# Performance work log

Measured on AMD Instinct MI355X. Metric: run time of the kernel, lower is better.

## Reference

```python
import jax, jax.numpy as jnp
from jax import lax
import numpy as np

B, T, F, U, O = 512, 512, 128, 256, 32  # batch, max_t, joint feature dim, lstm units, n_output


def setup_inputs() -> dict:
    key = jax.random.key(0)
    k = jax.random.split(key, 6)
    return {
        "x_joint": jax.random.normal(k[0], (B, T, F), dtype=jnp.float32),
        "Wx": jax.random.normal(k[1], (F, 4 * U), dtype=jnp.float32) / np.sqrt(F).astype(np.float32),
        "Wh": jax.random.normal(k[2], (U, 4 * U), dtype=jnp.float32) / np.sqrt(U).astype(np.float32),
        "b": jnp.zeros((4 * U,), dtype=jnp.float32),
        "Wo": jax.random.normal(k[3], (U, O), dtype=jnp.float32) / np.sqrt(U).astype(np.float32),
        "bo": jnp.zeros((O,), dtype=jnp.float32),
        "seq_lengths": jax.random.randint(k[4], (B,), 0, T, dtype=jnp.int32),
    }


def reference(x_joint, Wx, Wh, b, Wo, bo, seq_lengths):
    """Masked LSTM decoder scan with per-step Dense projection.

    Flax nn.RNN(DecoderLSTMCell): LSTMCell gates i,f,g,o then Dense(n_output).
    With return_carry=True + seq_lengths, flax only uses seq_lengths to slice the
    final carry, which RNNSurrogate discards; outputs are the full per-step
    predictions, so seq_lengths does not enter the returned math.
    """
    bsz, t, _ = x_joint.shape
    units = Wh.shape[0]
    # precompute input contribution to all 4 gates: [B, T, 4U]
    x_proj = jnp.einsum('btf,fg->btg', x_joint, Wx) + b
    c0 = jnp.zeros((bsz, units), dtype=x_joint.dtype)
    h0 = jnp.zeros((bsz, units), dtype=x_joint.dtype)

    def step(carry, xt):
        c, h = carry
        z = xt + h @ Wh  # [B, 4U]
        i, f, g, o = jnp.split(z, 4, axis=-1)
        c = jax.nn.sigmoid(f) * c + jax.nn.sigmoid(i) * jnp.tanh(g)
        h = jax.nn.sigmoid(o) * jnp.tanh(c)
        y = h @ Wo + bo  # per-step Dense projection
        return (c, h), y

    _, ys = lax.scan(step, (c0, h0), x_proj.transpose(1, 0, 2))  # ys: [T, B, O]
    return ys.transpose(1, 0, 2)  # [B, T, O]
```

## Files before the change

### kernel.cpp

```cpp
#include <hip/hip_runtime.h>
#include <stdint.h>

#define BB 512
#define TT 512
#define FF 128
#define UU 256

typedef float f32x4 __attribute__((ext_vector_type(4)));
typedef short short8 __attribute__((ext_vector_type(8)));
typedef int int4v __attribute__((ext_vector_type(4)));
typedef float float4v __attribute__((ext_vector_type(4)));
typedef unsigned short ushort4v __attribute__((ext_vector_type(4)));

__device__ __forceinline__ unsigned short f2bf(float f) {
  union { float f; uint32_t u; } v; v.f = f;
  uint32_t u = v.u;
  u += 0x7fffu + ((u >> 16) & 1u);
  return (unsigned short)(u >> 16);
}
__device__ __forceinline__ float fast_rcp(float x) { return __builtin_amdgcn_rcpf(x); }
__device__ __forceinline__ float sigmoidf_(float x) { return fast_rcp(1.f + __expf(-x)); }
__device__ __forceinline__ float tanhf_(float x) { return 1.f - 2.f * fast_rcp(1.f + __expf(2.f * x)); }

__global__ void prep_w(const float* __restrict__ Wx, const float* __restrict__ Wh,
                       const float* __restrict__ Wo,
                       unsigned short* __restrict__ Wt, unsigned short* __restrict__ Wot,
                       int* __restrict__ flags) {
  int bidx = blockIdx.x;
  int tid = threadIdx.x;
  if (bidx < 1024) {
    int n = bidx, k = tid;
    float v = (k < FF) ? Wx[(size_t)k * 1024 + n] : Wh[(size_t)(k - FF) * 1024 + n];
    Wt[(size_t)n * 384 + k] = f2bf(v);
  } else if (bidx == 1024) {
    for (int i = tid; i < 32 * 256; i += 384) {
      int o = i >> 8, u = i & 255;
      Wot[o * 256 + u] = f2bf(Wo[(size_t)u * 32 + o]);
    }
  } else {
    for (int i = tid; i < 64 * 32; i += 384)
      __hip_atomic_store(&flags[i], 0, __ATOMIC_RELAXED, __HIP_MEMORY_SCOPE_SYSTEM);
  }
}

__global__ void conv_x(const float* __restrict__ xf, unsigned short* __restrict__ xb) {
  size_t i = (size_t)blockIdx.x * 1024 + (size_t)threadIdx.x * 4;
  float4v v = *(const float4v*)(xf + i);
  ushort4v o;
  o.x = f2bf(v.x); o.y = f2bf(v.y); o.z = f2bf(v.z); o.w = f2bf(v.w);
  *(ushort4v*)(xb + i) = o;
}

__device__ __forceinline__ short8 load_xfrag(const unsigned short* p) {
  return *(const short8*)p;
}
__device__ __forceinline__ short8 load_xfrag(const float* p) {
  float4v lo = *(const float4v*)p;
  float4v hi = *(const float4v*)(p + 4);
  union { short8 v; unsigned short s[8]; } a;
  a.s[0] = f2bf(lo.x); a.s[1] = f2bf(lo.y); a.s[2] = f2bf(lo.z); a.s[3] = f2bf(lo.w);
  a.s[4] = f2bf(hi.x); a.s[5] = f2bf(hi.y); a.s[6] = f2bf(hi.z); a.s[7] = f2bf(hi.w);
  return a.v;
}

__device__ __forceinline__ void load4_coh(const unsigned short* p,
                                          short8& q0, short8& q1, short8& q2, short8& q3) {
  int4v a0, a1, a2, a3;
  asm volatile(
      "global_load_dwordx4 %0, %4, off sc0 sc1\n\t"
      "global_load_dwordx4 %1, %4, off offset:64 sc0 sc1\n\t"
      "global_load_dwordx4 %2, %4, off offset:128 sc0 sc1\n\t"
      "global_load_dwordx4 %3, %4, off offset:192 sc0 sc1\n\t"
      "s_waitcnt vmcnt(0)"
      : "=&v"(a0), "=&v"(a1), "=&v"(a2), "=&v"(a3) : "v"(p) : "memory");
  __builtin_amdgcn_sched_barrier(0);
  q0 = __builtin_bit_cast(short8, a0);
  q1 = __builtin_bit_cast(short8, a1);
  q2 = __builtin_bit_cast(short8, a2);
  q3 = __builtin_bit_cast(short8, a3);
}
__device__ __forceinline__ void store_coh_u16(unsigned short* p, unsigned short v) {
  asm volatile("global_store_short %0, %1, off sc0 sc1" :: "v"(p), "v"((uint32_t)v) : "memory");
}

template <int HALF, typename XT>
__device__ __forceinline__ void lstm_core(const XT* __restrict__ x,
                                          const unsigned short* __restrict__ Wt,
                                          const float* __restrict__ bvec,
                                          unsigned short* __restrict__ h_hist,
                                          int* flags, int bid, char* lds) {
  const int mt = bid & 31;
  const int partner = bid ^ 32;
  const int tid = threadIdx.x;
  const int w = tid >> 6, l = tid & 63;
  const int lr = l & 15, lhi = l >> 4;
  const int b0 = mt * 16;
  const int uloc = HALF * 128 + w * 16 + lr;
  char* hlds = lds + 131072;

#pragma unroll
  for (int g = 0; g < 4; ++g)
#pragma unroll
    for (int kk = 0; kk < 4; ++kk) {
      const unsigned short* wp = Wt + (size_t)(g * 256 + uloc) * 384 + kk * 32 + 8 * lhi;
      *(short8*)(lds + ((size_t)((w * 16 + g * 4 + kk) * 64 + l)) * 16) = *(const short8*)wp;
    }

  short8 Bh[4][8];
#pragma unroll
  for (int g = 0; g < 4; ++g) {
    const unsigned short* wp = Wt + (size_t)(g * 256 + uloc) * 384 + FF + 8 * lhi;
#pragma unroll
    for (int kf = 0; kf < 8; ++kf) Bh[g][kf] = *(const short8*)(wp + kf * 32);
  }
  float bias[4];
#pragma unroll
  for (int g = 0; g < 4; ++g) bias[g] = bvec[g * 256 + uloc];
  float cst[4] = {0.f, 0.f, 0.f, 0.f};

  constexpr int kf_own = HALF * 4;
  constexpr int kf_par = (1 - HALF) * 4;
  constexpr int kh_par = (1 - HALF) * 128;

  const int* fp = flags + partner * 32;

  short8 xa[4];
  {
    const XT* xp = x + ((size_t)(b0 + lr) * TT + 0) * FF + 8 * lhi;
#pragma unroll
    for (int kk = 0; kk < 4; ++kk) xa[kk] = load_xfrag(xp + kk * 32);
  }
  __syncthreads();

#pragma unroll 1
  for (int t = 0; t < TT; ++t) {
    const int cur = t & 1, nxt = cur ^ 1;

    f32x4 acc[4];
#pragma unroll
    for (int g = 0; g < 4; ++g) { f32x4 a4 = {bias[g], bias[g], bias[g], bias[g]}; acc[g] = a4; }

    if (t > 0) {
      short8 ho[4];
#pragma unroll
      for (int ko = 0; ko < 4; ++ko) {
        const int byte = cur * 4096 + lr * 256 + ((ko * 64 + lhi * 16) ^ ((lr & 7) << 4));
        ho[ko] = *(const short8*)(hlds + byte);
      }
#pragma unroll
      for (int ko = 0; ko < 4; ++ko)
#pragma unroll
        for (int g = 0; g < 4; ++g)
          acc[g] = __builtin_amdgcn_mfma_f32_16x16x32_bf16(ho[ko], Bh[g][kf_own + ko], acc[g], 0, 0, 0);
    }

#pragma unroll
    for (int kk = 0; kk < 4; ++kk) {
      short8 bx[4];
#pragma unroll
      for (int g = 0; g < 4; ++g)
        bx[g] = *(const short8*)(lds + ((size_t)((w * 16 + g * 4 + kk) * 64 + l)) * 16);
#pragma unroll
      for (int g = 0; g < 4; ++g)
        acc[g] = __builtin_amdgcn_mfma_f32_16x16x32_bf16(xa[kk], bx[g], acc[g], 0, 0, 0);
    }

    {
      const int tn = (t + 1 < TT) ? t + 1 : t;
      const XT* xp = x + ((size_t)(b0 + lr) * TT + tn) * FF + 8 * lhi;
#pragma unroll
      for (int kk = 0; kk < 4; ++kk) xa[kk] = load_xfrag(xp + kk * 32);
    }

    if (t > 0) {
      int fv;
      do {
        asm volatile("global_load_dword %0, %1, off sc0 sc1\n\ts_waitcnt vmcnt(0)"
                     : "=v"(fv) : "v"(fp) : "memory");
      } while (fv < t);
      __builtin_amdgcn_sched_barrier(0);

      const unsigned short* hpp =
          h_hist + (size_t)t * (BB * UU) + (size_t)(b0 + lr) * UU + 8 * lhi + kh_par;
      short8 hq0, hq1, hq2, hq3;
      load4_coh(hpp, hq0, hq1, hq2, hq3);
#pragma unroll
      for (int g = 0; g < 4; ++g) acc[g] = __builtin_amdgcn_mfma_f32_16x16x32_bf16(hq0, Bh[g][kf_par + 0], acc[g], 0, 0, 0);
#pragma unroll
      for (int g = 0; g < 4; ++g) acc[g] = __builtin_amdgcn_mfma_f32_16x16x32_bf16(hq1, Bh[g][kf_par + 1], acc[g], 0, 0, 0);
#pragma unroll
      for (int g = 0; g < 4; ++g) acc[g] = __builtin_amdgcn_mfma_f32_16x16x32_bf16(hq2, Bh[g][kf_par + 2], acc[g], 0, 0, 0);
#pragma unroll
      for (int g = 0; g < 4; ++g) acc[g] = __builtin_amdgcn_mfma_f32_16x16x32_bf16(hq3, Bh[g][kf_par + 3], acc[g], 0, 0, 0);
    }

    unsigned short hs[4];
#pragma unroll
    for (int r = 0; r < 4; ++r) {
      float zi = acc[0][r], zf = acc[1][r], zg = acc[2][r], zo = acc[3][r];
      float si = sigmoidf_(zi), sf = sigmoidf_(zf), so = sigmoidf_(zo);
      float tg = tanhf_(zg);
      float cn = sf * cst[r] + si * tg;
      cst[r] = cn;
      hs[r] = f2bf(so * tanhf_(cn));
    }

    unsigned short* hw = h_hist + (size_t)(t + 1) * (BB * UU) + uloc;
#pragma unroll
    for (int r = 0; r < 4; ++r) {
      const int row = 4 * lhi + r;
      const int byte = nxt * 4096 + row * 256 + (((w * 16 + lr) * 2) ^ ((row & 7) << 4));
      *(unsigned short*)(hlds + byte) = hs[r];
      store_coh_u16(hw + (size_t)(b0 + row) * UU, hs[r]);
    }

    asm volatile("s_waitcnt vmcnt(0)" ::: "memory");
    __syncthreads();
    if (tid == 0)
      __hip_atomic_store(&flags[bid * 32], t + 1, __ATOMIC_RELAXED, __HIP_MEMORY_SCOPE_SYSTEM);
  }
}

template <typename XT>
__global__ void __launch_bounds__(512, 2)
lstm_main7(const XT* __restrict__ x, const unsigned short* __restrict__ Wt,
           const float* __restrict__ bvec, unsigned short* __restrict__ h_hist, int* flags) {
  __shared__ __align__(16) char lds[139264];
  const int bid = blockIdx.x;
  if (bid < 32) lstm_core<0, XT>(x, Wt, bvec, h_hist, flags, bid, lds);
  else          lstm_core<1, XT>(x, Wt, bvec, h_hist, flags, bid, lds);
}

__global__ void __launch_bounds__(256)
y_gemm(const unsigned short* __restrict__ h_hist, const unsigned short* __restrict__ Wot,
       const float* __restrict__ bo, float* __restrict__ out) {
  int gw = (int)((blockIdx.x * 256 + threadIdx.x) >> 6);
  int l = threadIdx.x & 63;
  int lr = l & 15, lhi = l >> 4;
  int b = gw >> 5;
  int t0 = (gw & 31) * 16;

  short8 Wf[2][8];
#pragma unroll
  for (int n = 0; n < 2; ++n) {
    const unsigned short* wp = Wot + (n * 16 + lr) * 256 + 8 * lhi;
#pragma unroll
    for (int kk = 0; kk < 8; ++kk) Wf[n][kk] = *(const short8*)(wp + kk * 32);
  }
  f32x4 acc[2];
#pragma unroll
  for (int n = 0; n < 2; ++n) {
    float bb = bo[n * 16 + lr];
    f32x4 a4 = {bb, bb, bb, bb};
    acc[n] = a4;
  }
  const unsigned short* hp =
      h_hist + ((size_t)(t0 + lr + 1) * BB + b) * UU + 8 * lhi;
#pragma unroll
  for (int kk = 0; kk < 8; ++kk) {
    short8 a = *(const short8*)(hp + kk * 32);
#pragma unroll
    for (int n = 0; n < 2; ++n)
      acc[n] = __builtin_amdgcn_mfma_f32_16x16x32_bf16(a, Wf[n][kk], acc[n], 0, 0, 0);
  }
#pragma unroll
  for (int n = 0; n < 2; ++n) {
    int o = n * 16 + lr;
#pragma unroll
    for (int r = 0; r < 4; ++r) {
      int t = t0 + 4 * lhi + r;
      out[((size_t)b * TT + t) * 32 + o] = acc[n][r];
    }
  }
}

extern "C" void kernel_launch(void* const* d_in, const int* in_sizes, int n_in,
                              void* d_out, int out_size, void* d_ws, size_t ws_size,
                              hipStream_t stream) {
  const float* x  = (const float*)d_in[0];
  const float* Wx = (const float*)d_in[1];
  const float* Wh = (const float*)d_in[2];
  const float* bv = (const float*)d_in[3];
  const float* Wo = (const float*)d_in[4];
  const float* bo = (const float*)d_in[5];

  char* ws = (char*)d_ws;
  size_t off = 0;
  unsigned short* h_hist = (unsigned short*)(ws + off); off += (size_t)513 * BB * UU * 2;
  unsigned short* Wt384  = (unsigned short*)(ws + off); off += (size_t)1024 * 384 * 2;
  unsigned short* Wot    = (unsigned short*)(ws + off); off += (size_t)32 * 256 * 2;
  int* flags             = (int*)(ws + off);            off += (size_t)64 * 32 * 4;
  off = (off + 255) & ~(size_t)255;
  unsigned short* xb = (unsigned short*)(ws + off);
  const size_t need_xb = off + (size_t)BB * TT * FF * 2;

  prep_w<<<1026, 384, 0, stream>>>(Wx, Wh, Wo, Wt384, Wot, flags);
  if (ws_size >= need_xb) {
    conv_x<<<32768, 256, 0, stream>>>(x, xb);
    lstm_main7<unsigned short><<<64, 512, 0, stream>>>(xb, Wt384, bv, h_hist, flags);
  } else {
    lstm_main7<float><<<64, 512, 0, stream>>>(x, Wt384, bv, h_hist, flags);
  }
  y_gemm<<<4096, 256, 0, stream>>>(h_hist, Wot, bo, (float*)d_out);
}
```

Before: 1.799 ms.

## Embed step tags in exchanged h values, fuse output projection into LSTM

Partner blocks now exchange hidden state through a small double-buffered scratch area. Each 32-bit word packs a bf16 h value with the step number, so the consumer polls the data itself instead of waiting on a separate flag and then reading h_hist. This removes one round-trip of global latency per step, along with the trailing vmcnt wait and barrier-before-flag. The input projection for the next step is computed after the h store so it overlaps the partner's latency. The output Dense projection is fused into the recurrent kernel, which eliminates the full h history buffer and the separate y_gemm launch. The trade-off is double the exchange bytes (32-bit words instead of 16-bit) and extra MFMA work inside the serial loop.

```diff
diff --git a/kernel.cpp b/kernel.cpp
--- a/kernel.cpp
+++ b/kernel.cpp
@@ -25,7 +25,7 @@
 __global__ void prep_w(const float* __restrict__ Wx, const float* __restrict__ Wh,
                        const float* __restrict__ Wo,
                        unsigned short* __restrict__ Wt, unsigned short* __restrict__ Wot,
-                       int* __restrict__ flags) {
+                       int* __restrict__ xch) {
   int bidx = blockIdx.x;
   int tid = threadIdx.x;
   if (bidx < 1024) {
@@ -38,8 +38,8 @@
       Wot[o * 256 + u] = f2bf(Wo[(size_t)u * 32 + o]);
     }
   } else {
-    for (int i = tid; i < 64 * 32; i += 384)
-      __hip_atomic_store(&flags[i], 0, __ATOMIC_RELAXED, __HIP_MEMORY_SCOPE_SYSTEM);
+    int base = (bidx - 1025) * 2048;
+    for (int i = tid; i < 2048; i += 384) xch[base + i] = 0;
   }
 }
 
@@ -63,40 +63,63 @@
   return a.v;
 }
 
-__device__ __forceinline__ void load4_coh(const unsigned short* p,
-                                          short8& q0, short8& q1, short8& q2, short8& q3) {
-  int4v a0, a1, a2, a3;
-  asm volatile(
-      "global_load_dwordx4 %0, %4, off sc0 sc1\n\t"
-      "global_load_dwordx4 %1, %4, off offset:64 sc0 sc1\n\t"
-      "global_load_dwordx4 %2, %4, off offset:128 sc0 sc1\n\t"
-      "global_load_dwordx4 %3, %4, off offset:192 sc0 sc1\n\t"
-      "s_waitcnt vmcnt(0)"
-      : "=&v"(a0), "=&v"(a1), "=&v"(a2), "=&v"(a3) : "v"(p) : "memory");
+__device__ __forceinline__ void store_sc01(int* p, int v) {
+  asm volatile("global_store_dword %0, %1, off sc0 sc1" :: "v"(p), "v"(v) : "memory");
+}
+__device__ __forceinline__ int tchk(const int4v& v, int t) {
+  return ((v.x ^ t) | (v.y ^ t) | (v.z ^ t) | (v.w ^ t)) & 0xffff;
+}
+__device__ __forceinline__ uint32_t pk2(int lo, int hi) {
+  return ((uint32_t)lo >> 16) | ((uint32_t)hi & 0xffff0000u);
+}
+__device__ __forceinline__ short8 pack2(const int4v& a, const int4v& b) {
+  int4v k;
+  k.x = (int)pk2(a.x, a.y); k.y = (int)pk2(a.z, a.w);
+  k.z = (int)pk2(b.x, b.y); k.w = (int)pk2(b.z, b.w);
+  return __builtin_bit_cast(short8, k);
+}
+
+__device__ __forceinline__ void poll_hq(const int* pb, int t, short8* hq) {
+  int4v a0, a1, a2, a3, a4, a5, a6, a7;
+  for (;;) {
+    asm volatile(
+        "global_load_dwordx4 %0, %8, off sc0 sc1\n\t"
+        "global_load_dwordx4 %1, %8, off offset:16 sc0 sc1\n\t"
+        "global_load_dwordx4 %2, %8, off offset:128 sc0 sc1\n\t"
+        "global_load_dwordx4 %3, %8, off offset:144 sc0 sc1\n\t"
+        "global_load_dwordx4 %4, %8, off offset:256 sc0 sc1\n\t"
+        "global_load_dwordx4 %5, %8, off offset:272 sc0 sc1\n\t"
+        "global_load_dwordx4 %6, %8, off offset:384 sc0 sc1\n\t"
+        "global_load_dwordx4 %7, %8, off offset:400 sc0 sc1\n\t"
+        "s_waitcnt vmcnt(0)"
+        : "=&v"(a0), "=&v"(a1), "=&v"(a2), "=&v"(a3),
+          "=&v"(a4), "=&v"(a5), "=&v"(a6), "=&v"(a7)
+        : "v"(pb) : "memory");
+    int m = tchk(a0, t) | tchk(a1, t) | tchk(a2, t) | tchk(a3, t)
+          | tchk(a4, t) | tchk(a5, t) | tchk(a6, t) | tchk(a7, t);
+    if (__all(m == 0)) break;
+  }
   __builtin_amdgcn_sched_barrier(0);
-  q0 = __builtin_bit_cast(short8, a0);
-  q1 = __builtin_bit_cast(short8, a1);
-  q2 = __builtin_bit_cast(short8, a2);
-  q3 = __builtin_bit_cast(short8, a3);
-}
-__device__ __forceinline__ void store_coh_u16(unsigned short* p, unsigned short v) {
-  asm volatile("global_store_short %0, %1, off sc0 sc1" :: "v"(p), "v"((uint32_t)v) : "memory");
+  hq[0] = pack2(a0, a1); hq[1] = pack2(a2, a3);
+  hq[2] = pack2(a4, a5); hq[3] = pack2(a6, a7);
 }
 
 template <int HALF, typename XT>
 __device__ __forceinline__ void lstm_core(const XT* __restrict__ x,
                                           const unsigned short* __restrict__ Wt,
+                                          const unsigned short* __restrict__ Wot,
                                           const float* __restrict__ bvec,
-                                          unsigned short* __restrict__ h_hist,
-                                          int* flags, int bid, char* lds) {
+                                          const float* __restrict__ bo,
+                                          float* __restrict__ out,
+                                          int* __restrict__ xch, int bid, char* lds) {
   const int mt = bid & 31;
-  const int partner = bid ^ 32;
   const int tid = threadIdx.x;
   const int w = tid >> 6, l = tid & 63;
   const int lr = l & 15, lhi = l >> 4;
   const int b0 = mt * 16;
   const int uloc = HALF * 128 + w * 16 + lr;
-  char* hlds = lds + 131072;
+  char* h_lds  = lds + 131072;
+  char* wo_lds = lds + 139264;
 
 #pragma unroll
   for (int g = 0; g < 4; ++g)
@@ -105,6 +128,13 @@
       const unsigned short* wp = Wt + (size_t)(g * 256 + uloc) * 384 + kk * 32 + 8 * lhi;
       *(short8*)(lds + ((size_t)((w * 16 + g * 4 + kk) * 64 + l)) * 16) = *(const short8*)wp;
     }
+  if (w == 0) {
+#pragma unroll
+    for (int kf = 0; kf < 8; ++kf) {
+      const unsigned short* wp = Wot + (size_t)(HALF * 16 + lr) * 256 + kf * 32 + 8 * lhi;
+      *(short8*)(wo_lds + (size_t)(kf * 64 + l) * 16) = *(const short8*)wp;
+    }
+  }
 
   short8 Bh[4][8];
 #pragma unroll
@@ -116,21 +146,33 @@
   float bias[4];
 #pragma unroll
   for (int g = 0; g < 4; ++g) bias[g] = bvec[g * 256 + uloc];
+  const float bob = bo[HALF * 16 + lr];
   float cst[4] = {0.f, 0.f, 0.f, 0.f};
 
-  constexpr int kf_own = HALF * 4;
-  constexpr int kf_par = (1 - HALF) * 4;
-  constexpr int kh_par = (1 - HALF) * 128;
-
-  const int* fp = flags + partner * 32;
-
-  short8 xa[4];
+  const int rtile = (mt * 2 + (1 - HALF)) * 2;
+  const int wtile = (mt * 2 + HALF) * 2;
+  const int roff = lr * 128 + 8 * lhi;
+
+  f32x4 zx[4];
   {
+    short8 xa0[4];
     const XT* xp = x + ((size_t)(b0 + lr) * TT + 0) * FF + 8 * lhi;
 #pragma unroll
-    for (int kk = 0; kk < 4; ++kk) xa[kk] = load_xfrag(xp + kk * 32);
-  }
-  __syncthreads();
+    for (int kk = 0; kk < 4; ++kk) xa0[kk] = load_xfrag(xp + kk * 32);
+    __syncthreads();
+#pragma unroll
+    for (int g = 0; g < 4; ++g) { f32x4 a4 = {bias[g], bias[g], bias[g], bias[g]}; zx[g] = a4; }
+#pragma unroll
+    for (int kk = 0; kk < 4; ++kk) {
+      short8 bx[4];
+#pragma unroll
+      for (int g = 0; g < 4; ++g)
+        bx[g] = *(const short8*)(lds + ((size_t)((w * 16 + g * 4 + kk) * 64 + l)) * 16);
+#pragma unroll
+      for (int g = 0; g < 4; ++g)
+        zx[g] = __builtin_amdgcn_mfma_f32_16x16x32_bf16(xa0[kk], bx[g], zx[g], 0, 0, 0);
+    }
+  }
 
 #pragma unroll 1
   for (int t = 0; t < TT; ++t) {
@@ -138,60 +180,35 @@
 
     f32x4 acc[4];
 #pragma unroll
-    for (int g = 0; g < 4; ++g) { f32x4 a4 = {bias[g], bias[g], bias[g], bias[g]}; acc[g] = a4; }
-
-    if (t > 0) {
-      short8 ho[4];
-#pragma unroll
-      for (int ko = 0; ko < 4; ++ko) {
-        const int byte = cur * 4096 + lr * 256 + ((ko * 64 + lhi * 16) ^ ((lr & 7) << 4));
-        ho[ko] = *(const short8*)(hlds + byte);
-      }
-#pragma unroll
-      for (int ko = 0; ko < 4; ++ko)
-#pragma unroll
-        for (int g = 0; g < 4; ++g)
-          acc[g] = __builtin_amdgcn_mfma_f32_16x16x32_bf16(ho[ko], Bh[g][kf_own + ko], acc[g], 0, 0, 0);
-    }
-
-#pragma unroll
-    for (int kk = 0; kk < 4; ++kk) {
-      short8 bx[4];
-#pragma unroll
-      for (int g = 0; g < 4; ++g)
-        bx[g] = *(const short8*)(lds + ((size_t)((w * 16 + g * 4 + kk) * 64 + l)) * 16);
-#pragma unroll
-      for (int g = 0; g < 4; ++g)
-        acc[g] = __builtin_amdgcn_mfma_f32_16x16x32_bf16(xa[kk], bx[g], acc[g], 0, 0, 0);
-    }
-
+    for (int g = 0; g < 4; ++g) acc[g] = zx[g];
+
+    short8 xan[4];
     {
       const int tn = (t + 1 < TT) ? t + 1 : t;
       const XT* xp = x + ((size_t)(b0 + lr) * TT + tn) * FF + 8 * lhi;
 #pragma unroll
-      for (int kk = 0; kk < 4; ++kk) xa[kk] = load_xfrag(xp + kk * 32);
-    }
-
+      for (int kk = 0; kk < 4; ++kk) xan[kk] = load_xfrag(xp + kk * 32);
+    }
+
+    short8 ho[4], hq[4];
     if (t > 0) {
-      int fv;
-      do {
-        asm volatile("global_load_dword %0, %1, off sc0 sc1\n\ts_waitcnt vmcnt(0)"
-                     : "=v"(fv) : "v"(fp) : "memory");
-      } while (fv < t);
-      __builtin_amdgcn_sched_barrier(0);
-
-      const unsigned short* hpp =
-          h_hist + (size_t)t * (BB * UU) + (size_t)(b0 + lr) * UU + 8 * lhi + kh_par;
-      short8 hq0, hq1, hq2, hq3;
-      load4_coh(hpp, hq0, hq1, hq2, hq3);
-#pragma unroll
-      for (int g = 0; g < 4; ++g) acc[g] = __builtin_amdgcn_mfma_f32_16x16x32_bf16(hq0, Bh[g][kf_par + 0], acc[g], 0, 0, 0);
-#pragma unroll
-      for (int g = 0; g < 4; ++g) acc[g] = __builtin_amdgcn_mfma_f32_16x16x32_bf16(hq1, Bh[g][kf_par + 1], acc[g], 0, 0, 0);
-#pragma unroll
-      for (int g = 0; g < 4; ++g) acc[g] = __builtin_amdgcn_mfma_f32_16x16x32_bf16(hq2, Bh[g][kf_par + 2], acc[g], 0, 0, 0);
-#pragma unroll
-      for (int g = 0; g < 4; ++g) acc[g] = __builtin_amdgcn_mfma_f32_16x16x32_bf16(hq3, Bh[g][kf_par + 3], acc[g], 0, 0, 0);
+#pragma unroll
+      for (int ko = 0; ko < 4; ++ko) {
+        const int byte = cur * 4096 + lr * 256 + ((ko * 64 + lhi * 16) ^ ((lr & 7) << 4));
+        ho[ko] = *(const short8*)(h_lds + byte);
+      }
+#pragma unroll
+      for (int ko = 0; ko < 4; ++ko)
+#pragma unroll
+        for (int g = 0; g < 4; ++g)
+          acc[g] = __builtin_amdgcn_mfma_f32_16x16x32_bf16(ho[ko], Bh[g][HALF * 4 + ko], acc[g], 0, 0, 0);
+
+      poll_hq(xch + (rtile + cur) * 2048 + roff, t, hq);
+#pragma unroll
+      for (int kf = 0; kf < 4; ++kf)
+#pragma unroll
+        for (int g = 0; g < 4; ++g)
+          acc[g] = __builtin_amdgcn_mfma_f32_16x16x32_bf16(hq[kf], Bh[g][(1 - HALF) * 4 + kf], acc[g], 0, 0, 0);
     }
 
     unsigned short hs[4];
@@ -205,73 +222,81 @@
       hs[r] = f2bf(so * tanhf_(cn));
     }
 
-    unsigned short* hw = h_hist + (size_t)(t + 1) * (BB * UU) + uloc;
+    const int wb = (wtile + nxt) * 2048 + w * 16 + lr;
 #pragma unroll
     for (int r = 0; r < 4; ++r) {
       const int row = 4 * lhi + r;
       const int byte = nxt * 4096 + row * 256 + (((w * 16 + lr) * 2) ^ ((row & 7) << 4));
-      *(unsigned short*)(hlds + byte) = hs[r];
-      store_coh_u16(hw + (size_t)(b0 + row) * UU, hs[r]);
-    }
-
-    asm volatile("s_waitcnt vmcnt(0)" ::: "memory");
+      *(unsigned short*)(h_lds + byte) = hs[r];
+      store_sc01(xch + wb + row * 128, ((int)(uint32_t)hs[r] << 16) | (t + 1));
+    }
+
+#pragma unroll
+    for (int g = 0; g < 4; ++g) { f32x4 a4 = {bias[g], bias[g], bias[g], bias[g]}; zx[g] = a4; }
+#pragma unroll
+    for (int kk = 0; kk < 4; ++kk) {
+      short8 bx[4];
+#pragma unroll
+      for (int g = 0; g < 4; ++g)
+        bx[g] = *(const short8*)(lds + ((size_t)((w * 16 + g * 4 + kk) * 64 + l)) * 16);
+#pragma unroll
+      for (int g = 0; g < 4; ++g)
+        zx[g] = __builtin_amdgcn_mfma_f32_16x16x32_bf16(xan[kk], bx[g], zx[g], 0, 0, 0);
+    }
+    if (t > 0) {
+      f32x4 yacc = {bob, bob, bob, bob};
+#pragma unroll
+      for (int ko = 0; ko < 4; ++ko) {
+        short8 wo = *(const short8*)(wo_lds + (size_t)((HALF * 4 + ko) * 64 + l) * 16);
+        yacc = __builtin_amdgcn_mfma_f32_16x16x32_bf16(ho[ko], wo, yacc, 0, 0, 0);
+      }
+#pragma unroll
+      for (int kf = 0; kf < 4; ++kf) {
+        short8 wo = *(const short8*)(wo_lds + (size_t)(((1 - HALF) * 4 + kf) * 64 + l) * 16);
+        yacc = __builtin_amdgcn_mfma_f32_16x16x32_bf16(hq[kf], wo, yacc, 0, 0, 0);
+      }
+#pragma unroll
+      for (int r = 0; r < 4; ++r)
+        out[((size_t)(b0 + 4 * lhi + r) * TT + (t - 1)) * 32 + HALF * 16 + lr] = yacc[r];
+    }
+
     __syncthreads();
-    if (tid == 0)
-      __hip_atomic_store(&flags[bid * 32], t + 1, __ATOMIC_RELAXED, __HIP_MEMORY_SCOPE_SYSTEM);
+  }
+
+  {
+    short8 ho[4], hq[4];
+#pragma unroll
+    for (int ko = 0; ko < 4; ++ko) {
+      const int byte = 0 * 4096 + lr * 256 + ((ko * 64 + lhi * 16) ^ ((lr & 7) << 4));
+      ho[ko] = *(const short8*)(h_lds + byte);
+    }
+    poll_hq(xch + (rtile + 0) * 2048 + roff, TT, hq);
+    f32x4 yacc = {bob, bob, bob, bob};
+#pragma unroll
+    for (int ko = 0; ko < 4; ++ko) {
+      short8 wo = *(const short8*)(wo_lds + (size_t)((HALF * 4 + ko) * 64 + l) * 16);
+      yacc = __builtin_amdgcn_mfma_f32_16x16x32_bf16(ho[ko], wo, yacc, 0, 0, 0);
+    }
+#pragma unroll
+    for (int kf = 0; kf < 4; ++kf) {
+      short8 wo = *(const short8*)(wo_lds + (size_t)(((1 - HALF) * 4 + kf) * 64 + l) * 16);
+      yacc = __builtin_amdgcn_mfma_f32_16x16x32_bf16(hq[kf], wo, yacc, 0, 0, 0);
+    }
+#pragma unroll
+    for (int r = 0; r < 4; ++r)
+      out[((size_t)(b0 + 4 * lhi + r) * TT + (TT - 1)) * 32 + HALF * 16 + lr] = yacc[r];
   }
 }
 
 template <typename XT>
 __global__ void __launch_bounds__(512, 2)
-lstm_main7(const XT* __restrict__ x, const unsigned short* __restrict__ Wt,
-           const float* __restrict__ bvec, unsigned short* __restrict__ h_hist, int* flags) {
-  __shared__ __align__(16) char lds[139264];
+lstm_main8(const XT* __restrict__ x, const unsigned short* __restrict__ Wt,
+           const unsigned short* __restrict__ Wot, const float* __restrict__ bvec,
+           const float* __restrict__ bo, float* __restrict__ out, int* __restrict__ xch) {
+  __shared__ __align__(16) char lds[147456];
   const int bid = blockIdx.x;
-  if (bid < 32) lstm_core<0, XT>(x, Wt, bvec, h_hist, flags, bid, lds);
-  else          lstm_core<1, XT>(x, Wt, bvec, h_hist, flags, bid, lds);
-}
-
-__global__ void __launch_bounds__(256)
-y_gemm(const unsigned short* __restrict__ h_hist, const unsigned short* __restrict__ Wot,
-       const float* __restrict__ bo, float* __restrict__ out) {
-  int gw = (int)((blockIdx.x * 256 + threadIdx.x) >> 6);
-  int l = threadIdx.x & 63;
-  int lr = l & 15, lhi = l >> 4;
-  int b = gw >> 5;
-  int t0 = (gw & 31) * 16;
-
-  short8 Wf[2][8];
-#pragma unroll
-  for (int n = 0; n < 2; ++n) {
-    const unsigned short* wp = Wot + (n * 16 + lr) * 256 + 8 * lhi;
-#pragma unroll
-    for (int kk = 0; kk < 8; ++kk) Wf[n][kk] = *(const short8*)(wp + kk * 32);
-  }
-  f32x4 acc[2];
-#pragma unroll
-  for (int n = 0; n < 2; ++n) {
-    float bb = bo[n * 16 + lr];
-    f32x4 a4 = {bb, bb, bb, bb};
-    acc[n] = a4;
-  }
-  const unsigned short* hp =
-      h_hist + ((size_t)(t0 + lr + 1) * BB + b) * UU + 8 * lhi;
-#pragma unroll
-  for (int kk = 0; kk < 8; ++kk) {
-    short8 a = *(const short8*)(hp + kk * 32);
-#pragma unroll
-    for (int n = 0; n < 2; ++n)
-      acc[n] = __builtin_amdgcn_mfma_f32_16x16x32_bf16(a, Wf[n][kk], acc[n], 0, 0, 0);
-  }
-#pragma unroll
-  for (int n = 0; n < 2; ++n) {
-    int o = n * 16 + lr;
-#pragma unroll
-    for (int r = 0; r < 4; ++r) {
-      int t = t0 + 4 * lhi + r;
-      out[((size_t)b * TT + t) * 32 + o] = acc[n][r];
-    }
-  }
+  if (bid < 32) lstm_core<0, XT>(x, Wt, Wot, bvec, bo, out, xch, bid, lds);
+  else          lstm_core<1, XT>(x, Wt, Wot, bvec, bo, out, xch, bid, lds);
 }
 
 extern "C" void kernel_launch(void* const* d_in, const int* in_sizes, int n_in,
@@ -286,20 +311,18 @@
 
   char* ws = (char*)d_ws;
   size_t off = 0;
-  unsigned short* h_hist = (unsigned short*)(ws + off); off += (size_t)513 * BB * UU * 2;
-  unsigned short* Wt384  = (unsigned short*)(ws + off); off += (size_t)1024 * 384 * 2;
-  unsigned short* Wot    = (unsigned short*)(ws + off); off += (size_t)32 * 256 * 2;
-  int* flags             = (int*)(ws + off);            off += (size_t)64 * 32 * 4;
+  int* xch = (int*)(ws + off);                          off += (size_t)262144 * 4;
+  unsigned short* Wt384 = (unsigned short*)(ws + off);  off += (size_t)1024 * 384 * 2;
+  unsigned short* Wot   = (unsigned short*)(ws + off);  off += (size_t)32 * 256 * 2;
   off = (off + 255) & ~(size_t)255;
   unsigned short* xb = (unsigned short*)(ws + off);
   const size_t need_xb = off + (size_t)BB * TT * FF * 2;
 
-  prep_w<<<1026, 384, 0, stream>>>(Wx, Wh, Wo, Wt384, Wot, flags);
+  prep_w<<<1153, 384, 0, stream>>>(Wx, Wh, Wo, Wt384, Wot, xch);
   if (ws_size >= need_xb) {
     conv_x<<<32768, 256, 0, stream>>>(x, xb);
-    lstm_main7<unsigned short><<<64, 512, 0, stream>>>(xb, Wt384, bv, h_hist, flags);
+    lstm_main8<unsigned short><<<64, 512, 0, stream>>>(xb, Wt384, Wot, bv, bo, (float*)d_out, xch);
   } else {
-    lstm_main7<float><<<64, 512, 0, stream>>>(x, Wt384, bv, h_hist, flags);
-  }
-  y_gemm<<<4096, 256, 0, stream>>>(h_hist, Wot, bo, (float*)d_out);
-}
+    lstm_main8<float><<<64, 512, 0, stream>>>(x, Wt384, Wot, bv, bo, (float*)d_out, xch);
+  }
+}
```

Result: slower. 3.324 ms (+84.8%).

## Replace flag-based partner sync with tagged hidden-state exchange buffer

Applied to the files above, without the earlier changes.

Removes the separate per-block flag and the wait for store completion before signalling. Each hidden value is now written as a 32-bit word that packs the bf16 value with the step number into a double-buffered exchange area. The partner block polls that data directly until every tag matches the current step, then stages the values through LDS to build MFMA fragments. This cuts a full store-drain plus flag round trip from each step, in exchange for wider polling loads, an extra LDS pass and barrier, and reliance on tag correctness with 16-bit step counters.

```diff
diff --git a/kernel.cpp b/kernel.cpp
--- a/kernel.cpp
+++ b/kernel.cpp
@@ -25,7 +25,7 @@
 __global__ void prep_w(const float* __restrict__ Wx, const float* __restrict__ Wh,
                        const float* __restrict__ Wo,
                        unsigned short* __restrict__ Wt, unsigned short* __restrict__ Wot,
-                       int* __restrict__ flags) {
+                       int* __restrict__ xch) {
   int bidx = blockIdx.x;
   int tid = threadIdx.x;
   if (bidx < 1024) {
@@ -38,8 +38,8 @@
       Wot[o * 256 + u] = f2bf(Wo[(size_t)u * 32 + o]);
     }
   } else {
-    for (int i = tid; i < 64 * 32; i += 384)
-      __hip_atomic_store(&flags[i], 0, __ATOMIC_RELAXED, __HIP_MEMORY_SCOPE_SYSTEM);
+    int base = (bidx - 1025) * 2048;
+    for (int i = tid; i < 2048; i += 384) xch[base + i] = 0;
   }
 }
 
@@ -63,24 +63,11 @@
   return a.v;
 }
 
-__device__ __forceinline__ void load4_coh(const unsigned short* p,
-                                          short8& q0, short8& q1, short8& q2, short8& q3) {
-  int4v a0, a1, a2, a3;
-  asm volatile(
-      "global_load_dwordx4 %0, %4, off sc0 sc1\n\t"
-      "global_load_dwordx4 %1, %4, off offset:64 sc0 sc1\n\t"
-      "global_load_dwordx4 %2, %4, off offset:128 sc0 sc1\n\t"
-      "global_load_dwordx4 %3, %4, off offset:192 sc0 sc1\n\t"
-      "s_waitcnt vmcnt(0)"
-      : "=&v"(a0), "=&v"(a1), "=&v"(a2), "=&v"(a3) : "v"(p) : "memory");
-  __builtin_amdgcn_sched_barrier(0);
-  q0 = __builtin_bit_cast(short8, a0);
-  q1 = __builtin_bit_cast(short8, a1);
-  q2 = __builtin_bit_cast(short8, a2);
-  q3 = __builtin_bit_cast(short8, a3);
-}
-__device__ __forceinline__ void store_coh_u16(unsigned short* p, unsigned short v) {
-  asm volatile("global_store_short %0, %1, off sc0 sc1" :: "v"(p), "v"((uint32_t)v) : "memory");
+__device__ __forceinline__ void store_sc01(int* p, int v) {
+  asm volatile("global_store_dword %0, %1, off sc0 sc1" :: "v"(p), "v"(v) : "memory");
+}
+__device__ __forceinline__ uint32_t pk2(int lo, int hi) {
+  return ((uint32_t)lo >> 16) | ((uint32_t)hi & 0xffff0000u);
 }
 
 template <int HALF, typename XT>
@@ -88,15 +75,15 @@
                                           const unsigned short* __restrict__ Wt,
                                           const float* __restrict__ bvec,
                                           unsigned short* __restrict__ h_hist,
-                                          int* flags, int bid, char* lds) {
+                                          int* __restrict__ xch, int bid, char* lds) {
   const int mt = bid & 31;
-  const int partner = bid ^ 32;
   const int tid = threadIdx.x;
   const int w = tid >> 6, l = tid & 63;
   const int lr = l & 15, lhi = l >> 4;
   const int b0 = mt * 16;
   const int uloc = HALF * 128 + w * 16 + lr;
   char* hlds = lds + 131072;
+  char* plds = lds + 139264;
 
 #pragma unroll
   for (int g = 0; g < 4; ++g)
@@ -120,9 +107,12 @@
 
   constexpr int kf_own = HALF * 4;
   constexpr int kf_par = (1 - HALF) * 4;
-  constexpr int kh_par = (1 - HALF) * 128;
-
-  const int* fp = flags + partner * 32;
+
+  const int rtile = (mt * 2 + (1 - HALF)) * 2;
+  const int wtile = (mt * 2 + HALF) * 2;
+
+  const int prow = tid >> 5;
+  const int pwbyte = (prow * 256 + (tid & 31) * 8) ^ ((prow & 7) << 4);
 
   short8 xa[4];
   {
@@ -173,25 +163,31 @@
     }
 
     if (t > 0) {
-      int fv;
-      do {
-        asm volatile("global_load_dword %0, %1, off sc0 sc1\n\ts_waitcnt vmcnt(0)"
-                     : "=v"(fv) : "v"(fp) : "memory");
-      } while (fv < t);
+      const int* pp = xch + (rtile + cur) * 2048 + 4 * tid;
+      int4v a;
+      for (;;) {
+        asm volatile("global_load_dwordx4 %0, %1, off sc0 sc1\n\ts_waitcnt vmcnt(0)"
+                     : "=&v"(a) : "v"(pp) : "memory");
+        int m = ((a.x ^ t) | (a.y ^ t) | (a.z ^ t) | (a.w ^ t)) & 0xffff;
+        if (__all(m == 0)) break;
+      }
       __builtin_amdgcn_sched_barrier(0);
 
-      const unsigned short* hpp =
-          h_hist + (size_t)t * (BB * UU) + (size_t)(b0 + lr) * UU + 8 * lhi + kh_par;
-      short8 hq0, hq1, hq2, hq3;
-      load4_coh(hpp, hq0, hq1, hq2, hq3);
-#pragma unroll
-      for (int g = 0; g < 4; ++g) acc[g] = __builtin_amdgcn_mfma_f32_16x16x32_bf16(hq0, Bh[g][kf_par + 0], acc[g], 0, 0, 0);
-#pragma unroll
-      for (int g = 0; g < 4; ++g) acc[g] = __builtin_amdgcn_mfma_f32_16x16x32_bf16(hq1, Bh[g][kf_par + 1], acc[g], 0, 0, 0);
-#pragma unroll
-      for (int g = 0; g < 4; ++g) acc[g] = __builtin_amdgcn_mfma_f32_16x16x32_bf16(hq2, Bh[g][kf_par + 2], acc[g], 0, 0, 0);
-#pragma unroll
-      for (int g = 0; g < 4; ++g) acc[g] = __builtin_amdgcn_mfma_f32_16x16x32_bf16(hq3, Bh[g][kf_par + 3], acc[g], 0, 0, 0);
+      uint32_t d0 = pk2(a.x, a.y), d1 = pk2(a.z, a.w);
+      *(uint64_t*)(plds + pwbyte) = ((uint64_t)d1 << 32) | d0;
+      __syncthreads();
+
+      short8 hq[4];
+#pragma unroll
+      for (int ko = 0; ko < 4; ++ko) {
+        const int byte = (lr * 256 + lhi * 16 + ko * 64) ^ ((lr & 7) << 4);
+        hq[ko] = *(const short8*)(plds + byte);
+      }
+#pragma unroll
+      for (int ko = 0; ko < 4; ++ko)
+#pragma unroll
+        for (int g = 0; g < 4; ++g)
+          acc[g] = __builtin_amdgcn_mfma_f32_16x16x32_bf16(hq[ko], Bh[g][kf_par + ko], acc[g], 0, 0, 0);
     }
 
     unsigned short hs[4];
@@ -205,30 +201,30 @@
       hs[r] = f2bf(so * tanhf_(cn));
     }
 
+    const int wb = (wtile + nxt) * 2048 + w * 16 + lr;
     unsigned short* hw = h_hist + (size_t)(t + 1) * (BB * UU) + uloc;
 #pragma unroll
     for (int r = 0; r < 4; ++r) {
       const int row = 4 * lhi + r;
       const int byte = nxt * 4096 + row * 256 + (((w * 16 + lr) * 2) ^ ((row & 7) << 4));
       *(unsigned short*)(hlds + byte) = hs[r];
-      store_coh_u16(hw + (size_t)(b0 + row) * UU, hs[r]);
-    }
-
-    asm volatile("s_waitcnt vmcnt(0)" ::: "memory");
+      store_sc01(xch + wb + row * 128, ((int)(uint32_t)hs[r] << 16) | (t + 1));
+      hw[(size_t)(b0 + row) * UU] = hs[r];
+    }
+
     __syncthreads();
-    if (tid == 0)
-      __hip_atomic_store(&flags[bid * 32], t + 1, __ATOMIC_RELAXED, __HIP_MEMORY_SCOPE_SYSTEM);
   }
 }
 
 template <typename XT>
 __global__ void __launch_bounds__(512, 2)
-lstm_main7(const XT* __restrict__ x, const unsigned short* __restrict__ Wt,
-           const float* __restrict__ bvec, unsigned short* __restrict__ h_hist, int* flags) {
-  __shared__ __align__(16) char lds[139264];
+lstm_main10(const XT* __restrict__ x, const unsigned short* __restrict__ Wt,
+            const float* __restrict__ bvec, unsigned short* __restrict__ h_hist,
+            int* __restrict__ xch) {
+  __shared__ __align__(16) char lds[143360];
   const int bid = blockIdx.x;
-  if (bid < 32) lstm_core<0, XT>(x, Wt, bvec, h_hist, flags, bid, lds);
-  else          lstm_core<1, XT>(x, Wt, bvec, h_hist, flags, bid, lds);
+  if (bid < 32) lstm_core<0, XT>(x, Wt, bvec, h_hist, xch, bid, lds);
+  else          lstm_core<1, XT>(x, Wt, bvec, h_hist, xch, bid, lds);
 }
 
 __global__ void __launch_bounds__(256)
@@ -286,20 +282,20 @@
 
   char* ws = (char*)d_ws;
   size_t off = 0;
+  int* xch = (int*)(ws + off);                          off += (size_t)262144 * 4;
   unsigned short* h_hist = (unsigned short*)(ws + off); off += (size_t)513 * BB * UU * 2;
   unsigned short* Wt384  = (unsigned short*)(ws + off); off += (size_t)1024 * 384 * 2;
   unsigned short* Wot    = (unsigned short*)(ws + off); off += (size_t)32 * 256 * 2;
-  int* flags             = (int*)(ws + off);            off += (size_t)64 * 32 * 4;
   off = (off + 255) & ~(size_t)255;
   unsigned short* xb = (unsigned short*)(ws + off);
   const size_t need_xb = off + (size_t)BB * TT * FF * 2;
 
-  prep_w<<<1026, 384, 0, stream>>>(Wx, Wh, Wo, Wt384, Wot, flags);
+  prep_w<<<1153, 384, 0, stream>>>(Wx, Wh, Wo, Wt384, Wot, xch);
   if (ws_size >= need_xb) {
     conv_x<<<32768, 256, 0, stream>>>(x, xb);
-    lstm_main7<unsigned short><<<64, 512, 0, stream>>>(xb, Wt384, bv, h_hist, flags);
+    lstm_main10<unsigned short><<<64, 512, 0, stream>>>(xb, Wt384, bv, h_hist, xch);
   } else {
-    lstm_main7<float><<<64, 512, 0, stream>>>(x, Wt384, bv, h_hist, flags);
+    lstm_main10<float><<<64, 512, 0, stream>>>(x, Wt384, bv, h_hist, xch);
   }
   y_gemm<<<4096, 256, 0, stream>>>(h_hist, Wot, bo, (float*)d_out);
 }
```

Measured after the change: 1.483 ms, median of 2. 17.6% less time.
